# Kernel optimization log

Hardware: AMD Instinct MI355X
Metric: run time of the kernel (lower is better)

## Reference

```python
import jax, jax.numpy as jnp
import numpy as np

N = 50000
E = 800000
IN, HID, OUT = 128, 128, 64


def setup_inputs() -> dict:
    key = jax.random.key(0)
    ks = jax.random.split(key, 12)
    x = jax.random.normal(ks[0], (N, IN), dtype=jnp.float32)
    src = jax.random.randint(ks[1], (E,), 0, N)
    dst = jax.random.randint(ks[2], (E,), 0, N)
    edge_index = jnp.stack([src, dst]).astype(jnp.int64)
    def lin(k, fan_in, fan_out):
        s = 1.0 / np.sqrt(fan_in)
        return jax.random.uniform(k, (fan_in, fan_out), jnp.float32, -s, s)
    return {
        "x": x,
        "edge_index": edge_index,
        "w_l0": lin(ks[3], IN, HID), "b0": jnp.zeros((HID,), jnp.float32), "w_r0": lin(ks[4], IN, HID),
        "w_l1": lin(ks[5], HID, HID), "b1": jnp.zeros((HID,), jnp.float32), "w_r1": lin(ks[6], HID, HID),
        "w_l2": lin(ks[7], HID, OUT), "b2": jnp.zeros((OUT,), jnp.float32), "w_r2": lin(ks[8], HID, OUT),
    }


def _sage_conv(x, src, dst, w_l, b, w_r, num_nodes):
    # mean aggregation of source features onto destination nodes
    msg = x[src]                                            # [E, d]
    summed = jax.ops.segment_sum(msg, dst, num_segments=num_nodes)  # [N, d]
    deg = jax.ops.segment_sum(jnp.ones((src.shape[0],), x.dtype), dst, num_segments=num_nodes)
    aggr = summed / jnp.maximum(deg, 1.0)[:, None]
    # out = lin_l(aggr) + lin_r(x_root); bias only on lin_l (PyG SAGEConv default)
    return aggr @ w_l + b + x @ w_r


def reference(x, edge_index, w_l0, b0, w_r0, w_l1, b1, w_r1, w_l2, b2, w_r2):
    src, dst = edge_index[0].astype(jnp.int32), edge_index[1].astype(jnp.int32)
    n = x.shape[0]
    h = jax.nn.relu(_sage_conv(x, src, dst, w_l0, b0, w_r0, n))  # dropout: eval mode -> identity
    h = jax.nn.relu(_sage_conv(h, src, dst, w_l1, b1, w_r1, n))
    return _sage_conv(h, src, dst, w_l2, b2, w_r2, n)
```

## Files before the change

### kernel.cpp

```cpp
#include <hip/hip_runtime.h>
#include <cstdint>
#include <cstddef>


#define HID 128
#define NSLICE 8
#define FILL_BLOCKS_PER_SLICE 256
#define CAP 64

using short8 = __attribute__((ext_vector_type(8))) short;
using f32x4  = __attribute__((ext_vector_type(4))) float;


__device__ __forceinline__ unsigned short f32_to_bf16(float f)
{
    union { float f; unsigned int i; } c; c.f = f;
    const unsigned int x = c.i;
    const unsigned int r = x + 0x7fffu + ((x >> 16) & 1u);
    return (unsigned short)(r >> 16);
}

__device__ __forceinline__ float bf16_hi_to_f32(unsigned int hi16_in_low)
{
    union { unsigned int i; float f; } c; c.i = hi16_in_low << 16;
    return c.f;
}


#define PREP_THREADS (2 * 2 * HID * HID + 2 * 64 * HID)

__global__ __launch_bounds__(256) void prep_wt_zero_kernel(
    const float* __restrict__ wl0, const float* __restrict__ wr0,
    const float* __restrict__ wl1, const float* __restrict__ wr1,
    const float* __restrict__ wl2, const float* __restrict__ wr2,
    unsigned short* __restrict__ wt0, unsigned short* __restrict__ wt1,
    unsigned short* __restrict__ wt2, int* __restrict__ cnt, int n)
{
    const int idx = blockIdx.x * 256 + threadIdx.x;
    const int per128 = 2 * HID * HID;
    if (idx < per128) {
        const int k = idx & (HID - 1), c = idx >> 7;
        const float v = (c < HID) ? wl0[(size_t)k * HID + c] : wr0[(size_t)k * HID + (c - HID)];
        wt0[idx] = f32_to_bf16(v);
    } else if (idx < 2 * per128) {
        const int j = idx - per128;
        const int k = j & (HID - 1), c = j >> 7;
        const float v = (c < HID) ? wl1[(size_t)k * HID + c] : wr1[(size_t)k * HID + (c - HID)];
        wt1[j] = f32_to_bf16(v);
    } else if (idx < PREP_THREADS) {
        const int j = idx - 2 * per128;
        const int k = j & (HID - 1), c = j >> 7;
        const float v = (c < 64) ? wl2[(size_t)k * 64 + c] : wr2[(size_t)k * 64 + (c - 64)];
        wt2[j] = f32_to_bf16(v);
    } else {
        const int j = idx - PREP_THREADS;
        if (j < n) cnt[j] = 0;
    }
}


__global__ __launch_bounds__(256) void bucket_fill_sliced_kernel(
    const int* __restrict__ src, const int* __restrict__ dst,
    int* __restrict__ cnt, int* __restrict__ esrc, int E, int n)
{
    const int slice = blockIdx.x & (NSLICE - 1);
    const int nps   = (n + NSLICE - 1) / NSLICE;
    const int lo    = slice * nps;
    const int hi    = min(lo + nps, n);
    const int stride = FILL_BLOCKS_PER_SLICE * 256;
    int e = (blockIdx.x >> 3) * 256 + threadIdx.x;
    for (; e < E; e += stride) {
        const int d = dst[e];
        if (d >= lo && d < hi) {
            const int s = src[e];
            if ((unsigned)s < (unsigned)n) {
                const int p = atomicAdd(&cnt[d], 1);
                if (p < CAP) esrc[(size_t)d * CAP + p] = s;
            }
        }
    }
}


template <int DOUT, bool IN_F32, bool R_BF16>
__global__ __launch_bounds__(256) void sage_mfma_gemm(
    const void* __restrict__ hin,
    const unsigned short* __restrict__ wtc,
    const float* __restrict__ bias,
    unsigned short* __restrict__ p, void* __restrict__ r, int n)
{
    constexpr int TOTC = 2 * DOUT;
    constexpr int CPW  = TOTC / 64;

    const int tx   = threadIdx.x;
    const int wv   = tx >> 6;
    const int lane = tx & 63;
    const int quad = lane >> 4;
    const int l15  = lane & 15;

    short8 B[CPW][4];
#pragma unroll
    for (int t = 0; t < CPW; ++t) {
        const int c = (wv * CPW + t) * 16 + l15;
#pragma unroll
        for (int q = 0; q < 4; ++q)
            B[t][q] = *(const short8*)(wtc + (size_t)c * HID + q * 32 + quad * 8);
    }

    const int slabs = (n + 15) >> 4;
    for (int slab = blockIdx.x; slab < slabs; slab += gridDim.x) {
        const int r0 = slab * 16;
        const int rr = min(r0 + l15, n - 1);

        short8 A[4];
        if (IN_F32) {
            const float* hf = (const float*)hin;
#pragma unroll
            for (int q = 0; q < 4; ++q) {
                const float4 f0 = *(const float4*)(hf + (size_t)rr * HID + q * 32 + quad * 8);
                const float4 f1 = *(const float4*)(hf + (size_t)rr * HID + q * 32 + quad * 8 + 4);
                short8 a;
                a[0] = (short)f32_to_bf16(f0.x); a[1] = (short)f32_to_bf16(f0.y);
                a[2] = (short)f32_to_bf16(f0.z); a[3] = (short)f32_to_bf16(f0.w);
                a[4] = (short)f32_to_bf16(f1.x); a[5] = (short)f32_to_bf16(f1.y);
                a[6] = (short)f32_to_bf16(f1.z); a[7] = (short)f32_to_bf16(f1.w);
                A[q] = a;
            }
        } else {
            const unsigned short* hb = (const unsigned short*)hin;
#pragma unroll
            for (int q = 0; q < 4; ++q)
                A[q] = *(const short8*)(hb + (size_t)rr * HID + q * 32 + quad * 8);
        }

        f32x4 acc[CPW];
#pragma unroll
        for (int t = 0; t < CPW; ++t) acc[t] = (f32x4){0.f, 0.f, 0.f, 0.f};
#pragma unroll
        for (int q = 0; q < 4; ++q)
#pragma unroll
            for (int t = 0; t < CPW; ++t)
                acc[t] = __builtin_amdgcn_mfma_f32_16x16x32_bf16(A[q], B[t][q], acc[t], 0, 0, 0);

#pragma unroll
        for (int t = 0; t < CPW; ++t) {
            const int c0  = (wv * CPW + t) * 16;
            const int col = c0 + l15;
            if (c0 < DOUT) {
#pragma unroll
                for (int i = 0; i < 4; ++i) {
                    const int row = r0 + quad * 4 + i;
                    if (row < n) p[(size_t)row * DOUT + col] = f32_to_bf16(acc[t][i]);
                }
            } else {
                const float bv = bias[col - DOUT];
#pragma unroll
                for (int i = 0; i < 4; ++i) {
                    const int row = r0 + quad * 4 + i;
                    if (row < n) {
                        const float v = acc[t][i] + bv;
                        if (R_BF16)
                            ((unsigned short*)r)[(size_t)row * DOUT + (col - DOUT)] = f32_to_bf16(v);
                        else
                            ((float*)r)[(size_t)row * DOUT + (col - DOUT)] = v;
                    }
                }
            }
        }
    }
}


template <int DOUT, bool RELU, bool OUTBF16, bool R_BF16>
__global__ __launch_bounds__(256) void sage_post_aggregate(
    const unsigned short* __restrict__ p, const void* __restrict__ r,
    const int* __restrict__ cnt, const int* __restrict__ esrc,
    void* __restrict__ out, int n)
{
    const int wid  = threadIdx.x >> 6;
    const int lane = threadIdx.x & 63;
    const int node = blockIdx.x * 4 + wid;
    if (node >= n) return;
    const int dg   = cnt[node];
    const int degc = min(dg, CAP);
    const int beg  = node * CAP;
    const int end  = beg + degc;
    const float inv = 1.0f / fmaxf((float)dg, 1.0f);

    if constexpr (DOUT == 128) {
        float ax[8], ay[8];
#pragma unroll
        for (int j = 0; j < 8; ++j) { ax[j] = 0.f; ay[j] = 0.f; }
        for (int e = beg; e < end; e += 8) {
#pragma unroll
            for (int j = 0; j < 8; ++j) {
                const int idx = e + j;
                const int ee  = min(idx, end - 1);
                const float w = (idx < end) ? 1.0f : 0.0f;
                const int s   = esrc[ee];
                const unsigned int v = *(const unsigned int*)(&p[(size_t)s * DOUT + lane * 2]);
                ax[j] = fmaf(w, bf16_hi_to_f32(v & 0xffffu), ax[j]);
                ay[j] = fmaf(w, bf16_hi_to_f32(v >> 16), ay[j]);
            }
        }
        float sx = ((ax[0] + ax[1]) + (ax[2] + ax[3])) + ((ax[4] + ax[5]) + (ax[6] + ax[7]));
        float sy = ((ay[0] + ay[1]) + (ay[2] + ay[3])) + ((ay[4] + ay[5]) + (ay[6] + ay[7]));
        float rx, ry;
        if (R_BF16) {
            const unsigned int rv = ((const unsigned int*)r)[(size_t)node * (DOUT / 2) + lane];
            rx = bf16_hi_to_f32(rv & 0xffffu);
            ry = bf16_hi_to_f32(rv >> 16);
        } else {
            const float2 rv = *((const float2*)((const float*)r + (size_t)node * DOUT) + lane);
            rx = rv.x; ry = rv.y;
        }
        float ox = sx * inv + rx;
        float oy = sy * inv + ry;
        if (RELU) { ox = fmaxf(ox, 0.f); oy = fmaxf(oy, 0.f); }
        if (OUTBF16) {
            const unsigned int pk = ((unsigned int)f32_to_bf16(oy) << 16) | (unsigned int)f32_to_bf16(ox);
            ((unsigned int*)out)[(size_t)node * (DOUT / 2) + lane] = pk;
        } else {
            float2 o; o.x = ox; o.y = oy;
            *((float2*)((float*)out + (size_t)node * DOUT) + lane) = o;
        }
    } else {
        float a[8];
#pragma unroll
        for (int j = 0; j < 8; ++j) a[j] = 0.f;
        for (int e = beg; e < end; e += 8) {
#pragma unroll
            for (int j = 0; j < 8; ++j) {
                const int idx = e + j;
                const int ee  = min(idx, end - 1);
                const float w = (idx < end) ? 1.0f : 0.0f;
                const int s   = esrc[ee];
                const unsigned short u = p[(size_t)s * DOUT + lane];
                a[j] = fmaf(w, bf16_hi_to_f32((unsigned int)u), a[j]);
            }
        }
        float sa = ((a[0] + a[1]) + (a[2] + a[3])) + ((a[4] + a[5]) + (a[6] + a[7]));
        float rv;
        if (R_BF16) {
            const unsigned short u = ((const unsigned short*)r)[(size_t)node * DOUT + lane];
            rv = bf16_hi_to_f32((unsigned int)u);
        } else {
            rv = ((const float*)r)[(size_t)node * DOUT + lane];
        }
        float o = sa * inv + rv;
        if (RELU) o = fmaxf(o, 0.f);
        ((float*)out)[(size_t)node * DOUT + lane] = o;
    }
}


static inline size_t align_up(size_t v, size_t a) { return (v + a - 1) & ~(a - 1); }

extern "C" void kernel_launch(void* const* d_in, const int* in_sizes, int n_in,
                              void* d_out, int out_size, void* d_ws, size_t ws_size,
                              hipStream_t stream)
{
    const float* x   = (const float*)d_in[0];
    const int*   ei  = (const int*)d_in[1];
    const float* wl0 = (const float*)d_in[2];
    const float* b0  = (const float*)d_in[3];
    const float* wr0 = (const float*)d_in[4];
    const float* wl1 = (const float*)d_in[5];
    const float* b1  = (const float*)d_in[6];
    const float* wr1 = (const float*)d_in[7];
    const float* wl2 = (const float*)d_in[8];
    const float* b2  = (const float*)d_in[9];
    const float* wr2 = (const float*)d_in[10];
    float*       out = (float*)d_out;

    const int N = in_sizes[0] / HID;
    const int E = in_sizes[1] / 2;
    const int* src = ei;
    const int* dst = ei + E;

    char*  ws  = (char*)d_ws;
    size_t off = 0;
    int* cnt      = (int*)(ws + off); off = align_up(off + (size_t)N * 4, 256);
    int* esrc     = (int*)(ws + off); off = align_up(off + (size_t)N * CAP * 4, 256);
    unsigned short* pbuf = (unsigned short*)(ws + off); off = align_up(off + (size_t)N * HID * 2, 256);
    unsigned short* rb16 = (unsigned short*)(ws + off); off = align_up(off + (size_t)N * HID * 2, 256);
    float* rbf32  = (float*)(ws + off); off = align_up(off + (size_t)N * HID * 4, 256);
    unsigned short* hbf = (unsigned short*)(ws + off); off = align_up(off + (size_t)N * HID * 2, 256);
    unsigned short* wt0 = (unsigned short*)(ws + off); off = align_up(off + (size_t)2 * HID * HID * 2, 256);
    unsigned short* wt1 = (unsigned short*)(ws + off); off = align_up(off + (size_t)2 * HID * HID * 2, 256);
    unsigned short* wt2 = (unsigned short*)(ws + off); off = align_up(off + (size_t)HID * HID * 2, 256);
    (void)ws_size; (void)n_in; (void)out_size;

    prep_wt_zero_kernel<<<(PREP_THREADS + N + 255) / 256, 256, 0, stream>>>(
        wl0, wr0, wl1, wr1, wl2, wr2, wt0, wt1, wt2, cnt, N);

    bucket_fill_sliced_kernel<<<NSLICE * FILL_BLOCKS_PER_SLICE, 256, 0, stream>>>(
        src, dst, cnt, esrc, E, N);

    const int aggGrid  = (N + 3) / 4;
    const int gemmGrid = 1024;

    sage_mfma_gemm<128, true, true><<<gemmGrid, 256, 0, stream>>>(x, wt0, b0, pbuf, rb16, N);
    sage_post_aggregate<128, true, true, true><<<aggGrid, 256, 0, stream>>>(pbuf, rb16, cnt, esrc, hbf, N);

    sage_mfma_gemm<128, false, true><<<gemmGrid, 256, 0, stream>>>(hbf, wt1, b1, pbuf, rb16, N);
    sage_post_aggregate<128, true, true, true><<<aggGrid, 256, 0, stream>>>(pbuf, rb16, cnt, esrc, hbf, N);

    sage_mfma_gemm<64, false, false><<<gemmGrid, 256, 0, stream>>>(hbf, wt2, b2, pbuf, rbf32, N);
    sage_post_aggregate<64, false, false, false><<<aggGrid, 256, 0, stream>>>(pbuf, rbf32, cnt, esrc, out, N);
}
```

Before: 292.1 us.

## Pad per-node counters to separate lines and shuffle-broadcast edge sources

Each per-node degree counter now sits 32 ints apart, so atomics on neighbouring nodes no longer share a 128-byte line. This is meant to cut atomic contention in bucket fill. In aggregation, each wave loads all 64 bucket slots of source indices in one coalesced load and broadcasts them with __shfl, replacing per-edge scalar esrc loads. In exchange the counter array is 32x larger, so zeroing it and reading it are sparser, and the esrc loads also cover unused slots.

```diff
diff --git a/kernel.cpp b/kernel.cpp
--- a/kernel.cpp
+++ b/kernel.cpp
@@ -7,6 +7,7 @@
 #define NSLICE 8
 #define FILL_BLOCKS_PER_SLICE 256
 #define CAP 64
+#define CNT_STRIDE 32
 
 using short8 = __attribute__((ext_vector_type(8))) short;
 using f32x4  = __attribute__((ext_vector_type(4))) float;
@@ -54,7 +55,7 @@
         wt2[j] = f32_to_bf16(v);
     } else {
         const int j = idx - PREP_THREADS;
-        if (j < n) cnt[j] = 0;
+        if (j < n) cnt[(size_t)j * CNT_STRIDE] = 0;
     }
 }
 
@@ -74,7 +75,7 @@
         if (d >= lo && d < hi) {
             const int s = src[e];
             if ((unsigned)s < (unsigned)n) {
-                const int p = atomicAdd(&cnt[d], 1);
+                const int p = atomicAdd(&cnt[(size_t)d * CNT_STRIDE], 1);
                 if (p < CAP) esrc[(size_t)d * CAP + p] = s;
             }
         }
@@ -181,23 +182,22 @@
     const int lane = threadIdx.x & 63;
     const int node = blockIdx.x * 4 + wid;
     if (node >= n) return;
-    const int dg   = cnt[node];
+    const int dg   = cnt[(size_t)node * CNT_STRIDE];
     const int degc = min(dg, CAP);
-    const int beg  = node * CAP;
-    const int end  = beg + degc;
     const float inv = 1.0f / fmaxf((float)dg, 1.0f);
+
+    const int sidx = esrc[(size_t)node * CAP + lane];
 
     if constexpr (DOUT == 128) {
         float ax[8], ay[8];
 #pragma unroll
         for (int j = 0; j < 8; ++j) { ax[j] = 0.f; ay[j] = 0.f; }
-        for (int e = beg; e < end; e += 8) {
+        for (int e0 = 0; e0 < degc; e0 += 8) {
 #pragma unroll
             for (int j = 0; j < 8; ++j) {
-                const int idx = e + j;
-                const int ee  = min(idx, end - 1);
-                const float w = (idx < end) ? 1.0f : 0.0f;
-                const int s   = esrc[ee];
+                const int slot = e0 + j;
+                const float w  = (slot < degc) ? 1.0f : 0.0f;
+                const int s    = __shfl(sidx, min(slot, degc - 1), 64);
                 const unsigned int v = *(const unsigned int*)(&p[(size_t)s * DOUT + lane * 2]);
                 ax[j] = fmaf(w, bf16_hi_to_f32(v & 0xffffu), ax[j]);
                 ay[j] = fmaf(w, bf16_hi_to_f32(v >> 16), ay[j]);
@@ -228,13 +228,12 @@
         float a[8];
 #pragma unroll
         for (int j = 0; j < 8; ++j) a[j] = 0.f;
-        for (int e = beg; e < end; e += 8) {
+        for (int e0 = 0; e0 < degc; e0 += 8) {
 #pragma unroll
             for (int j = 0; j < 8; ++j) {
-                const int idx = e + j;
-                const int ee  = min(idx, end - 1);
-                const float w = (idx < end) ? 1.0f : 0.0f;
-                const int s   = esrc[ee];
+                const int slot = e0 + j;
+                const float w  = (slot < degc) ? 1.0f : 0.0f;
+                const int s    = __shfl(sidx, min(slot, degc - 1), 64);
                 const unsigned short u = p[(size_t)s * DOUT + lane];
                 a[j] = fmaf(w, bf16_hi_to_f32((unsigned int)u), a[j]);
             }
@@ -280,7 +279,7 @@
 
     char*  ws  = (char*)d_ws;
     size_t off = 0;
-    int* cnt      = (int*)(ws + off); off = align_up(off + (size_t)N * 4, 256);
+    int* cnt      = (int*)(ws + off); off = align_up(off + (size_t)N * CNT_STRIDE * 4, 256);
     int* esrc     = (int*)(ws + off); off = align_up(off + (size_t)N * CAP * 4, 256);
     unsigned short* pbuf = (unsigned short*)(ws + off); off = align_up(off + (size_t)N * HID * 2, 256);
     unsigned short* rb16 = (unsigned short*)(ws + off); off = align_up(off + (size_t)N * HID * 2, 256);
```

Result: faster. 283.4 us (-3.0%).
